# Kernel optimization log

Hardware: AMD Instinct MI355X
Metric: run time of the kernel (lower is better)

Reference implementation:

```python
import jax, jax.numpy as jnp
import numpy as np

DIM = 256
HEADS = 4
HEAD_DIM = DIM // HEADS
SCALE = HEAD_DIM ** -0.5


def setup_inputs() -> dict:
    key = jax.random.key(0)
    ks = jax.random.split(key, 9)
    B, N, C = 2, 4096, DIM
    x = jax.random.normal(ks[0], (B, N, C), dtype=jnp.float32)
    # xavier-uniform-ish init for square weights
    lim = np.sqrt(6.0 / (C + C)).astype(np.float32)
    def w(k):
        return jax.random.uniform(k, (C, C), dtype=jnp.float32, minval=-lim, maxval=lim)
    return {
        "x": x,
        "Wq": w(ks[1]), "bq": jnp.zeros((C,), jnp.float32),
        "Wk": w(ks[2]), "bk": jnp.zeros((C,), jnp.float32),
        "Wv": w(ks[3]), "bv": jnp.zeros((C,), jnp.float32),
        "Wo": w(ks[4]), "bo": jnp.zeros((C,), jnp.float32),
    }


def reference(x, Wq, bq, Wk, bk, Wv, bv, Wo, bo):
    B, N, C = x.shape
    x = jnp.clip(x, -10000.0, 10000.0)
    # projections (torch Linear: x @ W.T + b), then split heads -> [B, H, N, D]
    def heads(t):
        return t.reshape(B, N, HEADS, HEAD_DIM).transpose(0, 2, 1, 3)
    q = heads((x @ Wq.T + bq).astype(jnp.float32))
    k = heads((x @ Wk.T + bk).astype(jnp.float32))
    v = heads((x @ Wv.T + bv).astype(jnp.float32))
    # naive full attention: [B, H, N, N] scores materialized (as in source)
    attn = jnp.einsum("bhnd,bhmd->bhnm", q, k) * SCALE
    attn = jax.nn.softmax(attn, axis=-1)
    out = jnp.einsum("bhnm,bhmd->bhnd", attn, v)
    out = out.transpose(0, 2, 1, 3).reshape(B, N, C)
    # source casts to bf16 before the fp32 out_proj: emulate the precision loss
    out = out.astype(jnp.bfloat16).astype(jnp.float32)
    return out @ Wo.T + bo
```

## Files before the change

### kernel.cpp

```cpp
#include <hip/hip_runtime.h>
#include <hip/hip_bf16.h>

typedef unsigned short ushort_t;
typedef unsigned int u32;
typedef __bf16 bf16x4 __attribute__((ext_vector_type(4)));
typedef __bf16 bf16x8 __attribute__((ext_vector_type(8)));
typedef float f32x4 __attribute__((ext_vector_type(4)));
typedef float f32x16 __attribute__((ext_vector_type(16)));

#define DIMC 256
#define NSEQ 4096
#define BATCH 2
#define NHEADS 4
#define HDIM 64
#define QK_SCALE_LOG2E 0.18033688011112042f

__device__ __forceinline__ ushort_t f2bf(float f) {
    __bf16 b = (__bf16)f;
    return *(ushort_t*)&b;
}
__device__ __forceinline__ float clip1e4(float x) {
    return fminf(fmaxf(x, -10000.f), 10000.f);
}
__device__ __forceinline__ void gload_lds16(const void* g, void* l) {
    __builtin_amdgcn_global_load_lds((const __attribute__((address_space(1))) u32*)g,
                                     (__attribute__((address_space(3))) u32*)l, 16, 0, 0);
}

__global__ __launch_bounds__(256)
void qkv_proj_kernel(const float* __restrict__ xg,
                     const float* __restrict__ Wq, const float* __restrict__ bq,
                     const float* __restrict__ Wk, const float* __restrict__ bk,
                     const float* __restrict__ Wv, const float* __restrict__ bv,
                     ushort_t* __restrict__ Qg, ushort_t* __restrict__ Kg,
                     ushort_t* __restrict__ Vtg)
{
    __shared__ __attribute__((aligned(16))) ushort_t Ash[128][72];
    __shared__ __attribute__((aligned(16))) ushort_t Bsh[64][72];
    const int tid = threadIdx.x;
    const int lane = tid & 63;
    const int wv = tid >> 6;
    const int c16 = lane & 15;
    const int g = lane >> 4;

    const int bx = blockIdx.x;
    const int rowbase = blockIdx.y * 128;
    const int t = bx >> 2;
    const int cw = (bx & 3) * 64;

    const float* Wg = (t == 0) ? Wq : (t == 1) ? Wk : Wv;
    const float* bg = (t == 0) ? bq : (t == 1) ? bk : bv;
    const float cscale = (t == 0) ? QK_SCALE_LOG2E : 1.0f;

    const f32x4 zero = {0.f, 0.f, 0.f, 0.f};
    f32x4 acc[2][4];
#pragma unroll
    for (int a = 0; a < 2; ++a)
#pragma unroll
        for (int b = 0; b < 4; ++b) acc[a][b] = zero;

    for (int kt = 0; kt < 4; ++kt) {
        const int kb = kt * 64;
#pragma unroll
        for (int i = 0; i < 8; ++i) {
            int idx = tid + i * 256;
            int row = idx >> 4, c4 = (idx & 15) * 4;
            const float4 v = *(const float4*)&xg[(rowbase + row) * DIMC + kb + c4];
            bf16x4 pk;
            pk[0] = (__bf16)clip1e4(v.x); pk[1] = (__bf16)clip1e4(v.y);
            pk[2] = (__bf16)clip1e4(v.z); pk[3] = (__bf16)clip1e4(v.w);
            *(bf16x4*)&Ash[row][c4] = pk;
        }
#pragma unroll
        for (int i = 0; i < 4; ++i) {
            int idx = tid + i * 256;
            int row = idx >> 4, c4 = (idx & 15) * 4;
            const float4 v = *(const float4*)&Wg[(cw + row) * DIMC + kb + c4];
            bf16x4 pk;
            pk[0] = (__bf16)v.x; pk[1] = (__bf16)v.y;
            pk[2] = (__bf16)v.z; pk[3] = (__bf16)v.w;
            *(bf16x4*)&Bsh[row][c4] = pk;
        }
        __syncthreads();
#pragma unroll
        for (int ks = 0; ks < 2; ++ks) {
            bf16x8 a0 = *(const bf16x8*)&Ash[wv * 32 + c16][ks * 32 + g * 8];
            bf16x8 a1 = *(const bf16x8*)&Ash[wv * 32 + 16 + c16][ks * 32 + g * 8];
#pragma unroll
            for (int j = 0; j < 4; ++j) {
                bf16x8 bfr = *(const bf16x8*)&Bsh[j * 16 + c16][ks * 32 + g * 8];
                acc[0][j] = __builtin_amdgcn_mfma_f32_16x16x32_bf16(a0, bfr, acc[0][j], 0, 0, 0);
                acc[1][j] = __builtin_amdgcn_mfma_f32_16x16x32_bf16(a1, bfr, acc[1][j], 0, 0, 0);
            }
        }
        __syncthreads();
    }
    if (t < 2) {
        ushort_t* outg = (t == 0) ? Qg : Kg;
#pragma unroll
        for (int j = 0; j < 4; ++j) {
            int col = cw + j * 16 + c16;
            float bias = bg[col];
            int h = col >> 6, d = col & 63;
#pragma unroll
            for (int fr = 0; fr < 2; ++fr) {
#pragma unroll
                for (int r = 0; r < 4; ++r) {
                    int row = rowbase + wv * 32 + fr * 16 + g * 4 + r;
                    int b = row >> 12, n = row & (NSEQ - 1);
                    float val = (acc[fr][j][r] + bias) * cscale;
                    outg[(((b * NHEADS + h) * NSEQ) + n) * HDIM + d] = f2bf(val);
                }
            }
        }
    } else {
#pragma unroll
        for (int j = 0; j < 4; ++j) {
            int col = cw + j * 16 + c16;
            float bias = bg[col];
            int h = col >> 6, d = col & 63;
#pragma unroll
            for (int fr = 0; fr < 2; ++fr) {
                int row0 = rowbase + wv * 32 + fr * 16 + g * 4;
                int b = row0 >> 12, n0 = row0 & (NSEQ - 1);
                bf16x4 pk;
#pragma unroll
                for (int r = 0; r < 4; ++r) pk[r] = (__bf16)(acc[fr][j][r] + bias);
                *(bf16x4*)&Vtg[(((size_t)(b * NHEADS + h) << 6) + d) * NSEQ + n0] = pk;
            }
        }
    }
}

__global__ __launch_bounds__(256, 4)
void attn_kernel(const ushort_t* __restrict__ Qg, const ushort_t* __restrict__ Kg,
                 const ushort_t* __restrict__ Vtg, ushort_t* __restrict__ Op,
                 float* __restrict__ Lg)
{
    __shared__ __attribute__((aligned(16))) ushort_t pool[16384];
    __shared__ float Lsh[2][64];
    ushort_t* Kpool = pool;
    ushort_t* Vpool = pool + 8192;

    const int tid = threadIdx.x;
    const int lane = tid & 63;
    const int w = tid >> 6;
    const int l31 = lane & 31;
    const int hi = lane >> 5;
    const int qh = w & 1;
    const int kh = w >> 1;
    const int bh = blockIdx.x;
    const int qbase = blockIdx.y * 64;
    const int split = blockIdx.z;
    const int sub = lane >> 3, ch = lane & 7;

    bf16x8 qf[4];
    const int qrow = qbase + 32 * qh + l31;
#pragma unroll
    for (int m = 0; m < 4; ++m)
        qf[m] = *(const bf16x8*)&Qg[((bh * NSEQ + qrow) << 6) + 16 * m + hi * 8];

    f32x16 o[2];
#pragma unroll
    for (int n = 0; n < 2; ++n)
#pragma unroll
        for (int r = 0; r < 16; ++r) o[n][r] = 0.f;
    float lsum = 0.f;

    auto stageK = [&](int ta, int buf) {
#pragma unroll
        for (int i = 0; i < 2; ++i) {
            int row = w * 16 + i * 8 + sub;
            int chs = ch ^ (row & 7);
            gload_lds16(&Kg[((bh * NSEQ + ta * 64 + row) << 6) + chs * 8],
                        &Kpool[(buf * 64 + w * 16 + i * 8) * 64]);
        }
    };
    auto stageV = [&](int ta, int buf) {
#pragma unroll
        for (int i = 0; i < 2; ++i) {
            int row = w * 16 + i * 8 + sub;
            int chs = ch ^ (row & 7);
            gload_lds16(&Vtg[((bh << 6) + row) * NSEQ + ta * 64 + chs * 8],
                        &Vpool[(buf * 64 + w * 16 + i * 8) * 64]);
        }
    };

    const int t0 = split * 32;
    stageK(t0, 0);
    stageV(t0, 0);
    __syncthreads();

    for (int t = 0; t < 32; ++t) {
        const int cur = t & 1;
        if (t + 1 < 32) { stageK(t0 + t + 1, cur ^ 1); stageV(t0 + t + 1, cur ^ 1); }
        __builtin_amdgcn_sched_barrier(0);

        f32x16 s;
#pragma unroll
        for (int r = 0; r < 16; ++r) s[r] = 0.f;
        {
            const int krow = 32 * kh + l31, ksw = krow & 7;
#pragma unroll
            for (int m = 0; m < 4; ++m) {
                bf16x8 kf = *(const bf16x8*)&Kpool[(cur * 64 + krow) * 64 + ((2 * m + hi) ^ ksw) * 8];
                s = __builtin_amdgcn_mfma_f32_32x32x16_bf16(kf, qf[m], s, 0, 0, 0);
            }
        }

        u32 WA[4], WB[4];
#pragma unroll
        for (int g = 0; g < 4; ++g) {
            float e0 = exp2f(s[4 * g + 0]), e1 = exp2f(s[4 * g + 1]);
            float e2 = exp2f(s[4 * g + 2]), e3 = exp2f(s[4 * g + 3]);
            lsum += (e0 + e1) + (e2 + e3);
            asm("v_cvt_pk_bf16_f32 %0, %1, %2" : "=v"(WA[g]) : "v"(e0), "v"(e1));
            asm("v_cvt_pk_bf16_f32 %0, %1, %2" : "=v"(WB[g]) : "v"(e2), "v"(e3));
        }

#pragma unroll
        for (int m = 0; m < 2; ++m) {
            u32 a = WA[2 * m], b2 = WA[2 * m + 1];
            u32 c = WB[2 * m], d2 = WB[2 * m + 1];
            asm volatile("v_permlane32_swap_b32 %0, %1" : "+v"(a), "+v"(b2));
            asm volatile("v_permlane32_swap_b32 %0, %1" : "+v"(c), "+v"(d2));
            union { u32 u[4]; bf16x8 v; } pf;
            pf.u[0] = a; pf.u[1] = c; pf.u[2] = b2; pf.u[3] = d2;
#pragma unroll
            for (int n = 0; n < 2; ++n) {
                int vrow = 32 * n + l31;
                bf16x8 vf = *(const bf16x8*)
                    &Vpool[(cur * 64 + vrow) * 64 + ((4 * kh + 2 * m + hi) ^ (vrow & 7)) * 8];
                o[n] = __builtin_amdgcn_mfma_f32_32x32x16_bf16(pf.v, vf, o[n], 0, 0, 0);
            }
        }
        __syncthreads();
    }

    lsum += __shfl_xor(lsum, 32, 64);
    if (hi == 0) Lsh[kh][32 * qh + l31] = lsum;
    float* Red = (float*)pool;
    const int rbase = (qh * 64 + lane) * 34;
    if (kh == 1) {
#pragma unroll
        for (int n = 0; n < 2; ++n)
#pragma unroll
            for (int j = 0; j < 8; ++j) {
                float2 r; r.x = o[n][2 * j]; r.y = o[n][2 * j + 1];
                *(float2*)&Red[rbase + n * 16 + 2 * j] = r;
            }
    }
    __syncthreads();
    if (kh == 0) {
        const int b = bh >> 2, h = bh & 3;
#pragma unroll
        for (int n = 0; n < 2; ++n)
#pragma unroll
            for (int j = 0; j < 8; ++j) {
                float2 r = *(const float2*)&Red[rbase + n * 16 + 2 * j];
                o[n][2 * j] += r.x; o[n][2 * j + 1] += r.y;
            }
#pragma unroll
        for (int n = 0; n < 2; ++n)
#pragma unroll
            for (int reg = 0; reg < 16; ++reg) {
                int q = (reg & 3) + 8 * (reg >> 2) + 4 * hi + 32 * qh;
                Op[((size_t)(split * BATCH + b) * NSEQ + qbase + q) * DIMC
                   + h * HDIM + 32 * n + l31] = f2bf(o[n][reg]);
            }
        if (hi == 0) {
            int q = 32 * qh + l31;
            Lg[(split * 8 + bh) * NSEQ + qbase + q] = Lsh[0][q] + Lsh[1][q];
        }
    }
}

__global__ __launch_bounds__(256)
void oproj_kernel(const ushort_t* __restrict__ Op, const float* __restrict__ Lg,
                  const float* __restrict__ Wo, const float* __restrict__ bo,
                  float* __restrict__ outg)
{
    __shared__ __attribute__((aligned(16))) ushort_t Ash[128][72];
    __shared__ __attribute__((aligned(16))) ushort_t Bsh[64][72];
    const int tid = threadIdx.x;
    const int lane = tid & 63;
    const int wv = tid >> 6;
    const int c16 = lane & 15;
    const int g = lane >> 4;
    const int cw = blockIdx.x * 64;
    const int rowbase = blockIdx.y * 128;

    const f32x4 zero = {0.f, 0.f, 0.f, 0.f};
    f32x4 acc[2][4];
#pragma unroll
    for (int a = 0; a < 2; ++a)
#pragma unroll
        for (int b = 0; b < 4; ++b) acc[a][b] = zero;

    for (int kt = 0; kt < 4; ++kt) {
        const int kb = kt * 64;
#pragma unroll
        for (int i = 0; i < 4; ++i) {
            int idx = tid + i * 256;
            int row = idx >> 3, ch8 = (idx & 7) * 8;
            int grow = rowbase + row;
            int b = grow >> 12, n = grow & (NSEQ - 1);
            float l = Lg[(b * 4 + kt) * NSEQ + n] + Lg[(8 + b * 4 + kt) * NSEQ + n];
            float inv = 1.0f / l;
            bf16x8 O0 = *(const bf16x8*)&Op[((size_t)b * NSEQ + n) * DIMC + kb + ch8];
            bf16x8 O1 = *(const bf16x8*)&Op[((size_t)(BATCH + b) * NSEQ + n) * DIMC + kb + ch8];
            bf16x8 pk;
#pragma unroll
            for (int e = 0; e < 8; ++e)
                pk[e] = (__bf16)(((float)O0[e] + (float)O1[e]) * inv);
            *(bf16x8*)&Ash[row][ch8] = pk;
        }
#pragma unroll
        for (int i = 0; i < 4; ++i) {
            int idx = tid + i * 256;
            int row = idx >> 4, c4 = (idx & 15) * 4;
            const float4 v = *(const float4*)&Wo[(cw + row) * DIMC + kb + c4];
            bf16x4 pk;
            pk[0] = (__bf16)v.x; pk[1] = (__bf16)v.y;
            pk[2] = (__bf16)v.z; pk[3] = (__bf16)v.w;
            *(bf16x4*)&Bsh[row][c4] = pk;
        }
        __syncthreads();
#pragma unroll
        for (int ks = 0; ks < 2; ++ks) {
            bf16x8 a0 = *(const bf16x8*)&Ash[wv * 32 + c16][ks * 32 + g * 8];
            bf16x8 a1 = *(const bf16x8*)&Ash[wv * 32 + 16 + c16][ks * 32 + g * 8];
#pragma unroll
            for (int j = 0; j < 4; ++j) {
                bf16x8 bfr = *(const bf16x8*)&Bsh[j * 16 + c16][ks * 32 + g * 8];
                acc[0][j] = __builtin_amdgcn_mfma_f32_16x16x32_bf16(a0, bfr, acc[0][j], 0, 0, 0);
                acc[1][j] = __builtin_amdgcn_mfma_f32_16x16x32_bf16(a1, bfr, acc[1][j], 0, 0, 0);
            }
        }
        __syncthreads();
    }
#pragma unroll
    for (int j = 0; j < 4; ++j) {
        int col = cw + j * 16 + c16;
        float bias = bo[col];
#pragma unroll
        for (int fr = 0; fr < 2; ++fr) {
#pragma unroll
            for (int r = 0; r < 4; ++r) {
                int row = rowbase + wv * 32 + fr * 16 + g * 4 + r;
                outg[row * DIMC + col] = acc[fr][j][r] + bias;
            }
        }
    }
}

extern "C" void kernel_launch(void* const* d_in, const int* in_sizes, int n_in,
                              void* d_out, int out_size, void* d_ws, size_t ws_size,
                              hipStream_t stream)
{
    const float* x  = (const float*)d_in[0];
    const float* Wq = (const float*)d_in[1];
    const float* bq = (const float*)d_in[2];
    const float* Wk = (const float*)d_in[3];
    const float* bk = (const float*)d_in[4];
    const float* Wv = (const float*)d_in[5];
    const float* bv = (const float*)d_in[6];
    const float* Wo = (const float*)d_in[7];
    const float* bo = (const float*)d_in[8];
    float* out = (float*)d_out;

    ushort_t* ws = (ushort_t*)d_ws;
    const size_t SZ = (size_t)BATCH * NHEADS * NSEQ * HDIM;
    ushort_t* Qg  = ws;
    ushort_t* Kg  = ws + SZ;
    ushort_t* Vtg = ws + 2 * SZ;
    ushort_t* Op  = ws + 3 * SZ;
    float*    Lg  = (float*)(ws + 5 * SZ);

    qkv_proj_kernel<<<dim3(12, 64), 256, 0, stream>>>(x, Wq, bq, Wk, bk, Wv, bv, Qg, Kg, Vtg);
    attn_kernel<<<dim3(8, 64, 2), 256, 0, stream>>>(Qg, Kg, Vtg, Op, Lg);
    oproj_kernel<<<dim3(4, 64), 256, 0, stream>>>(Op, Lg, Wo, bo, out);
}
```

Measured before the change: 154.8 us.

## Give each wave full key tiles over 128-query blocks and drop the reduction

The attention kernel now assigns each of the four waves its own 32 query rows across all 64 keys of a tile, so a block covers 128 queries instead of 64. Previously pairs of waves split the keys and combined their partial outputs through shared memory. That LDS reduction and its extra barrier are gone, and each loaded K/V tile now serves twice as many queries, halving the grid. Address arithmetic for staging and reads is hoisted into running pointers. The trade-off is more accumulator registers per wave (launch bounds lowered to 2 blocks per CU) and fewer blocks, which reduces parallelism.

New measurement: 154.3 us. No clear change (-0.3%).

```diff
diff --git a/kernel.cpp b/kernel.cpp
--- a/kernel.cpp
+++ b/kernel.cpp
@@ -132,13 +132,12 @@
     }
 }
 
-__global__ __launch_bounds__(256, 4)
+__global__ __launch_bounds__(256, 2)
 void attn_kernel(const ushort_t* __restrict__ Qg, const ushort_t* __restrict__ Kg,
                  const ushort_t* __restrict__ Vtg, ushort_t* __restrict__ Op,
                  float* __restrict__ Lg)
 {
     __shared__ __attribute__((aligned(16))) ushort_t pool[16384];
-    __shared__ float Lsh[2][64];
     ushort_t* Kpool = pool;
     ushort_t* Vpool = pool + 8192;
 
@@ -147,131 +146,108 @@
     const int w = tid >> 6;
     const int l31 = lane & 31;
     const int hi = lane >> 5;
-    const int qh = w & 1;
-    const int kh = w >> 1;
     const int bh = blockIdx.x;
-    const int qbase = blockIdx.y * 64;
+    const int qbase = blockIdx.y * 128;
     const int split = blockIdx.z;
     const int sub = lane >> 3, ch = lane & 7;
 
     bf16x8 qf[4];
-    const int qrow = qbase + 32 * qh + l31;
+    const int qrow = qbase + 32 * w + l31;
 #pragma unroll
     for (int m = 0; m < 4; ++m)
         qf[m] = *(const bf16x8*)&Qg[((bh * NSEQ + qrow) << 6) + 16 * m + hi * 8];
 
-    f32x16 o[2];
-#pragma unroll
-    for (int n = 0; n < 2; ++n)
-#pragma unroll
-        for (int r = 0; r < 16; ++r) o[n][r] = 0.f;
+    f32x16 o0, o1;
+    f32x16 fz;
+#pragma unroll
+    for (int r = 0; r < 16; ++r) fz[r] = 0.f;
+    o0 = fz; o1 = fz;
     float lsum = 0.f;
 
-    auto stageK = [&](int ta, int buf) {
-#pragma unroll
-        for (int i = 0; i < 2; ++i) {
-            int row = w * 16 + i * 8 + sub;
-            int chs = ch ^ (row & 7);
-            gload_lds16(&Kg[((bh * NSEQ + ta * 64 + row) << 6) + chs * 8],
-                        &Kpool[(buf * 64 + w * 16 + i * 8) * 64]);
-        }
-    };
-    auto stageV = [&](int ta, int buf) {
-#pragma unroll
-        for (int i = 0; i < 2; ++i) {
-            int row = w * 16 + i * 8 + sub;
-            int chs = ch ^ (row & 7);
-            gload_lds16(&Vtg[((bh << 6) + row) * NSEQ + ta * 64 + chs * 8],
-                        &Vpool[(buf * 64 + w * 16 + i * 8) * 64]);
-        }
-    };
-
-    const int t0 = split * 32;
-    stageK(t0, 0);
-    stageV(t0, 0);
+    const ushort_t* Kp = Kg + (((size_t)bh * NSEQ + split * (NSEQ / 2) + w * 16 + sub) << 6)
+                            + (ch ^ sub) * 8;
+    const ushort_t* Vp  = Vtg + ((size_t)((bh << 6) + w * 16 + sub)) * NSEQ
+                              + split * (NSEQ / 2) + (ch ^ sub) * 8;
+    const ushort_t* Vp2 = Vp + 8 * NSEQ;
+    ushort_t* kd = Kpool + (w * 16) * 64;
+    ushort_t* vd = Vpool + (w * 16) * 64;
+
+    gload_lds16(Kp, kd);
+    gload_lds16(Kp + 512, kd + 512);
+    gload_lds16(Vp, vd);
+    gload_lds16(Vp2, vd + 512);
+    Kp += 4096; Vp += 64; Vp2 += 64;
     __syncthreads();
 
-    for (int t = 0; t < 32; ++t) {
+    const int ksw = l31 & 7;
+    const ushort_t* Krd  = Kpool + l31 * 64;
+    const ushort_t* Vrd0 = Vpool + l31 * 64;
+    const ushort_t* Vrd1 = Vpool + (32 + l31) * 64;
+
+    const int NT = NSEQ / 2 / 64;
+    for (int t = 0; t < NT; ++t) {
         const int cur = t & 1;
-        if (t + 1 < 32) { stageK(t0 + t + 1, cur ^ 1); stageV(t0 + t + 1, cur ^ 1); }
+        if (t + 1 < NT) {
+            const int nb = (t + 1) & 1;
+            gload_lds16(Kp, kd + nb * 4096);
+            gload_lds16(Kp + 512, kd + nb * 4096 + 512);
+            gload_lds16(Vp, vd + nb * 4096);
+            gload_lds16(Vp2, vd + nb * 4096 + 512);
+            Kp += 4096; Vp += 64; Vp2 += 64;
+        }
         __builtin_amdgcn_sched_barrier(0);
 
-        f32x16 s;
-#pragma unroll
-        for (int r = 0; r < 16; ++r) s[r] = 0.f;
-        {
-            const int krow = 32 * kh + l31, ksw = krow & 7;
-#pragma unroll
-            for (int m = 0; m < 4; ++m) {
-                bf16x8 kf = *(const bf16x8*)&Kpool[(cur * 64 + krow) * 64 + ((2 * m + hi) ^ ksw) * 8];
-                s = __builtin_amdgcn_mfma_f32_32x32x16_bf16(kf, qf[m], s, 0, 0, 0);
-            }
-        }
-
-        u32 WA[4], WB[4];
-#pragma unroll
-        for (int g = 0; g < 4; ++g) {
-            float e0 = exp2f(s[4 * g + 0]), e1 = exp2f(s[4 * g + 1]);
-            float e2 = exp2f(s[4 * g + 2]), e3 = exp2f(s[4 * g + 3]);
-            lsum += (e0 + e1) + (e2 + e3);
-            asm("v_cvt_pk_bf16_f32 %0, %1, %2" : "=v"(WA[g]) : "v"(e0), "v"(e1));
-            asm("v_cvt_pk_bf16_f32 %0, %1, %2" : "=v"(WB[g]) : "v"(e2), "v"(e3));
-        }
-
-#pragma unroll
-        for (int m = 0; m < 2; ++m) {
-            u32 a = WA[2 * m], b2 = WA[2 * m + 1];
-            u32 c = WB[2 * m], d2 = WB[2 * m + 1];
-            asm volatile("v_permlane32_swap_b32 %0, %1" : "+v"(a), "+v"(b2));
-            asm volatile("v_permlane32_swap_b32 %0, %1" : "+v"(c), "+v"(d2));
-            union { u32 u[4]; bf16x8 v; } pf;
-            pf.u[0] = a; pf.u[1] = c; pf.u[2] = b2; pf.u[3] = d2;
-#pragma unroll
-            for (int n = 0; n < 2; ++n) {
-                int vrow = 32 * n + l31;
-                bf16x8 vf = *(const bf16x8*)
-                    &Vpool[(cur * 64 + vrow) * 64 + ((4 * kh + 2 * m + hi) ^ (vrow & 7)) * 8];
-                o[n] = __builtin_amdgcn_mfma_f32_32x32x16_bf16(pf.v, vf, o[n], 0, 0, 0);
+        const int cb = cur * 4096;
+
+        f32x16 s0, s1;
+#pragma unroll
+        for (int m = 0; m < 4; ++m) {
+            bf16x8 kf0 = *(const bf16x8*)(Krd + cb + (((2 * m + hi) ^ ksw) * 8));
+            bf16x8 kf1 = *(const bf16x8*)(Krd + cb + 2048 + (((2 * m + hi) ^ ksw) * 8));
+            s0 = __builtin_amdgcn_mfma_f32_32x32x16_bf16(kf0, qf[m], m ? s0 : fz, 0, 0, 0);
+            s1 = __builtin_amdgcn_mfma_f32_32x32x16_bf16(kf1, qf[m], m ? s1 : fz, 0, 0, 0);
+        }
+
+#pragma unroll
+        for (int kb2 = 0; kb2 < 2; ++kb2) {
+            const f32x16& s = kb2 ? s1 : s0;
+            u32 WA[4], WB[4];
+#pragma unroll
+            for (int g = 0; g < 4; ++g) {
+                float e0 = exp2f(s[4 * g + 0]), e1 = exp2f(s[4 * g + 1]);
+                float e2 = exp2f(s[4 * g + 2]), e3 = exp2f(s[4 * g + 3]);
+                lsum += (e0 + e1) + (e2 + e3);
+                asm("v_cvt_pk_bf16_f32 %0, %1, %2" : "=v"(WA[g]) : "v"(e0), "v"(e1));
+                asm("v_cvt_pk_bf16_f32 %0, %1, %2" : "=v"(WB[g]) : "v"(e2), "v"(e3));
+            }
+#pragma unroll
+            for (int m2 = 0; m2 < 2; ++m2) {
+                u32 a = WA[2 * m2], b2 = WA[2 * m2 + 1];
+                u32 c = WB[2 * m2], d2 = WB[2 * m2 + 1];
+                asm volatile("v_permlane32_swap_b32 %0, %1" : "+v"(a), "+v"(b2));
+                asm volatile("v_permlane32_swap_b32 %0, %1" : "+v"(c), "+v"(d2));
+                union { u32 u[4]; bf16x8 v; } pf;
+                pf.u[0] = a; pf.u[1] = c; pf.u[2] = b2; pf.u[3] = d2;
+                const int vch = ((2 * (2 * kb2 + m2) + hi) ^ ksw) * 8;
+                bf16x8 vf0 = *(const bf16x8*)(Vrd0 + cb + vch);
+                bf16x8 vf1 = *(const bf16x8*)(Vrd1 + cb + vch);
+                o0 = __builtin_amdgcn_mfma_f32_32x32x16_bf16(pf.v, vf0, o0, 0, 0, 0);
+                o1 = __builtin_amdgcn_mfma_f32_32x32x16_bf16(pf.v, vf1, o1, 0, 0, 0);
             }
         }
         __syncthreads();
     }
 
     lsum += __shfl_xor(lsum, 32, 64);
-    if (hi == 0) Lsh[kh][32 * qh + l31] = lsum;
-    float* Red = (float*)pool;
-    const int rbase = (qh * 64 + lane) * 34;
-    if (kh == 1) {
-#pragma unroll
-        for (int n = 0; n < 2; ++n)
-#pragma unroll
-            for (int j = 0; j < 8; ++j) {
-                float2 r; r.x = o[n][2 * j]; r.y = o[n][2 * j + 1];
-                *(float2*)&Red[rbase + n * 16 + 2 * j] = r;
-            }
-    }
-    __syncthreads();
-    if (kh == 0) {
-        const int b = bh >> 2, h = bh & 3;
-#pragma unroll
-        for (int n = 0; n < 2; ++n)
-#pragma unroll
-            for (int j = 0; j < 8; ++j) {
-                float2 r = *(const float2*)&Red[rbase + n * 16 + 2 * j];
-                o[n][2 * j] += r.x; o[n][2 * j + 1] += r.y;
-            }
-#pragma unroll
-        for (int n = 0; n < 2; ++n)
-#pragma unroll
-            for (int reg = 0; reg < 16; ++reg) {
-                int q = (reg & 3) + 8 * (reg >> 2) + 4 * hi + 32 * qh;
-                Op[((size_t)(split * BATCH + b) * NSEQ + qbase + q) * DIMC
-                   + h * HDIM + 32 * n + l31] = f2bf(o[n][reg]);
-            }
-        if (hi == 0) {
-            int q = 32 * qh + l31;
-            Lg[(split * 8 + bh) * NSEQ + qbase + q] = Lsh[0][q] + Lsh[1][q];
-        }
+    const int b = bh >> 2, h = bh & 3;
+    if (hi == 0)
+        Lg[(split * 8 + bh) * NSEQ + qbase + 32 * w + l31] = lsum;
+#pragma unroll
+    for (int reg = 0; reg < 16; ++reg) {
+        int q = qbase + 32 * w + (reg & 3) + 8 * (reg >> 2) + 4 * hi;
+        size_t base = ((size_t)(split * BATCH + b) * NSEQ + q) * DIMC + h * HDIM;
+        Op[base + l31] = f2bf(o0[reg]);
+        Op[base + 32 + l31] = f2bf(o1[reg]);
     }
 }
 
@@ -378,6 +354,6 @@
     float*    Lg  = (float*)(ws + 5 * SZ);
 
     qkv_proj_kernel<<<dim3(12, 64), 256, 0, stream>>>(x, Wq, bq, Wk, bk, Wv, bv, Qg, Kg, Vtg);
-    attn_kernel<<<dim3(8, 64, 2), 256, 0, stream>>>(Qg, Kg, Vtg, Op, Lg);
+    attn_kernel<<<dim3(8, 32, 2), 256, 0, stream>>>(Qg, Kg, Vtg, Op, Lg);
     oproj_kernel<<<dim3(4, 64), 256, 0, stream>>>(Op, Lg, Wo, bo, out);
 }
```
